# Performance work log

Measured on AMD Instinct MI355X. Metric: run time of the kernel, lower is better.

## Reference

```python
import jax, jax.numpy as jnp
import numpy as np

B, S, D = 2, 2048, 1024
DIM_Q = DIM_V = 1024
N_HEAD = 16
NORM = 1.0 / np.sqrt(DIM_Q)


def setup_inputs() -> dict:
    key = jax.random.key(0)
    ks = jax.random.split(key, 12)
    inp = {
        'q': jax.random.normal(ks[0], (B, S, D), jnp.float32),
        'k': jax.random.normal(ks[1], (B, S, D), jnp.float32),
        'v': jax.random.normal(ks[2], (B, S, D), jnp.float32),
        'attn_mask': jnp.zeros((1, 1, S, S), jnp.float32),
        # Linear weights stored torch-style: (out_features, in_features)
        'wq_w': jax.random.normal(ks[3], (DIM_Q, D), jnp.float32) * 0.02,
        'wq_b': jnp.zeros((DIM_Q,), jnp.float32),
        'wk_w': jax.random.normal(ks[4], (DIM_Q, D), jnp.float32) * 0.02,
        'wk_b': jnp.zeros((DIM_Q,), jnp.float32),
        'wv_w': jax.random.normal(ks[5], (DIM_V, D), jnp.float32) * 0.02,
        'wv_b': jnp.zeros((DIM_V,), jnp.float32),
        'wo_w': jax.random.normal(ks[6], (DIM_V, DIM_V), jnp.float32) * 0.02,
        'wo_b': jnp.zeros((DIM_V,), jnp.float32),
    }
    return inp


def reference(q, k, v, attn_mask, wq_w, wq_b, wk_w, wk_b, wv_w, wv_b, wo_w, wo_b):
    dh_k = DIM_Q // N_HEAD
    dh_v = DIM_V // N_HEAD
    Q = q @ wq_w.T + wq_b                     # [B,S,DQ]
    K = k @ wk_w.T + wk_b                     # [B,S,DQ]
    V = v @ wv_w.T + wv_b                     # [B,S,DV]
    # Faithful to the original: raw reshape (no transpose) to [B, H, S, dh]
    Q = Q.reshape(B, N_HEAD, S, dh_k)
    K = K.reshape(B, N_HEAD, S, dh_k)
    V = V.reshape(B, N_HEAD, S, dh_v)
    att = jnp.einsum('bhqd,bhkd->bhqk', Q, K) * NORM
    att = att + attn_mask
    att = jax.nn.softmax(att, axis=-1)        # dropout is identity (eval)
    out = jnp.einsum('bhqk,bhkd->bhqd', att, V).reshape(B, S, DIM_V)
    out = out @ wo_w.T + wo_b                 # [B,S,DV]
    return out
```

## Files before the change

### kernel.cpp

```cpp
#include <hip/hip_runtime.h>
#include <stdint.h>

#define S_LEN 2048
#define DMODEL 1024
#define DH 64
#define MROWS 4096
#define NORM 0.03125f
#define QSCALE 0.045084439f

typedef __bf16 bf16x8 __attribute__((ext_vector_type(8)));
typedef float f32x4 __attribute__((ext_vector_type(4)));
typedef float f32x16 __attribute__((ext_vector_type(16)));

__device__ __forceinline__ uint16_t f2bf(float f) {
  union { float f; uint32_t u; } c; c.f = f;
  uint32_t u = c.u;
  u += 0x7fffu + ((u >> 16) & 1u);
  return (uint16_t)(u >> 16);
}

__device__ __forceinline__ void gload_lds16(const void* g, void* l) {
  __builtin_amdgcn_global_load_lds(
      (__attribute__((address_space(1))) void*)g,
      (__attribute__((address_space(3))) void*)l, 16, 0, 0);
}

struct CvtArgs {
  const float* src[7];
  uint16_t* dst[7];
  float scale[7];
  int n[7];
};

__global__ void cvt_bf16_kernel(CvtArgs a) {
  const int y = blockIdx.y;
  const float* __restrict__ src = a.src[y];
  uint16_t* __restrict__ dst = a.dst[y];
  const float sc = a.scale[y];
  const int n = a.n[y];
  int i = (blockIdx.x * blockDim.x + threadIdx.x) * 4;
  const int stride = gridDim.x * blockDim.x * 4;
  for (; i < n; i += stride) {
    float4 f = *reinterpret_cast<const float4*>(src + i);
    ushort4 o;
    o.x = f2bf(f.x * sc); o.y = f2bf(f.y * sc); o.z = f2bf(f.z * sc); o.w = f2bf(f.w * sc);
    *reinterpret_cast<ushort4*>(dst + i) = o;
  }
}

struct GemmBatch {
  const uint16_t* A[3];
  const uint16_t* W[3];
  const float* bias[3];
  float bscale[3];
  void* C[3];
};

template <bool OUT_F32, int NBT>
__global__ __launch_bounds__(256) void gemm_bt_kernel(GemmBatch args, int K) {
  const int BN = 32 * NBT;
  const int z = blockIdx.z;
  const uint16_t* __restrict__ A = args.A[z];
  const uint16_t* __restrict__ W = args.W[z];
  const float* __restrict__ bias = args.bias[z];
  const float bsc = args.bscale[z];

  __shared__ uint16_t Al[2][128 * 32];
  __shared__ uint16_t Bl[2][32 * NBT * 32];

  const int tid = threadIdx.x;
  const int w = tid >> 6, l = tid & 63;
  const int wm = w >> 1, wn = w & 1;
  const int li = l & 15, lg = l >> 4;
  const int m0 = blockIdx.y * 128, n0 = blockIdx.x * BN;

  const f32x4 zero4 = {0.f, 0.f, 0.f, 0.f};
  f32x4 acc[4][NBT];
#pragma unroll
  for (int mt = 0; mt < 4; ++mt)
#pragma unroll
    for (int nt = 0; nt < NBT; ++nt) acc[mt][nt] = zero4;

  const int srow = l >> 2;
  const int sc = (l & 3) * 8;

  const int nsteps = K >> 5;

  {
    const uint16_t* Ag = A + (size_t)m0 * K;
    const uint16_t* Wg = W + (size_t)n0 * K;
#pragma unroll
    for (int i = 0; i < 2; ++i) {
      const int rr = (w * 2 + i) * 16 + srow;
      gload_lds16(Ag + (size_t)rr * K + sc, &Al[0][(w * 2 + i) * 512]);
    }
#pragma unroll
    for (int i = 0; i < BN / 64; ++i) {
      const int rr = (w * (BN / 64) + i) * 16 + srow;
      gload_lds16(Wg + (size_t)rr * K + sc, &Bl[0][(w * (BN / 64) + i) * 512]);
    }
  }
  __syncthreads();

#pragma unroll 2
  for (int kt = 0; kt < nsteps; ++kt) {
    const int cur = kt & 1;
    if (kt + 1 < nsteps) {
      const uint16_t* Ag = A + (size_t)m0 * K + (kt + 1) * 32;
      const uint16_t* Wg = W + (size_t)n0 * K + (kt + 1) * 32;
#pragma unroll
      for (int i = 0; i < 2; ++i) {
        const int rr = (w * 2 + i) * 16 + srow;
        gload_lds16(Ag + (size_t)rr * K + sc, &Al[cur ^ 1][(w * 2 + i) * 512]);
      }
#pragma unroll
      for (int i = 0; i < BN / 64; ++i) {
        const int rr = (w * (BN / 64) + i) * 16 + srow;
        gload_lds16(Wg + (size_t)rr * K + sc, &Bl[cur ^ 1][(w * (BN / 64) + i) * 512]);
      }
    }

    bf16x8 af[4], bfv[NBT];
#pragma unroll
    for (int mt = 0; mt < 4; ++mt)
      af[mt] = *reinterpret_cast<const bf16x8*>(&Al[cur][(wm * 64 + mt * 16 + li) * 32 + lg * 8]);
#pragma unroll
    for (int nt = 0; nt < NBT; ++nt)
      bfv[nt] = *reinterpret_cast<const bf16x8*>(&Bl[cur][(wn * (NBT * 16) + nt * 16 + li) * 32 + lg * 8]);
#pragma unroll
    for (int mt = 0; mt < 4; ++mt)
#pragma unroll
      for (int nt = 0; nt < NBT; ++nt)
        acc[mt][nt] = __builtin_amdgcn_mfma_f32_16x16x32_bf16(af[mt], bfv[nt], acc[mt][nt], 0, 0, 0);
    __syncthreads();
  }

  const int rowbase = m0 + wm * 64;
  const int colbase = n0 + wn * (NBT * 16);
#pragma unroll
  for (int nt = 0; nt < NBT; ++nt) {
    const int col = colbase + nt * 16 + li;
    const float bv = bias[col] * bsc;
#pragma unroll
    for (int mt = 0; mt < 4; ++mt) {
#pragma unroll
      for (int r = 0; r < 4; ++r) {
        const int row = rowbase + mt * 16 + lg * 4 + r;
        const float v = acc[mt][nt][r] + bv;
        if constexpr (OUT_F32)
          reinterpret_cast<float*>(args.C[z])[(size_t)row * DMODEL + col] = v;
        else
          reinterpret_cast<uint16_t*>(args.C[z])[(size_t)row * DMODEL + col] = f2bf(v);
      }
    }
  }
}

__global__ __launch_bounds__(256) void vt_kernel(const uint16_t* __restrict__ Vp,
                                                 uint16_t* __restrict__ VT) {
  const int chunk = blockIdx.y;
  const int kt = blockIdx.x;
  const size_t cbase = (size_t)chunk * (S_LEN * DH);
  __shared__ uint16_t T[64 * 72];

  const int tid = threadIdx.x;
  const int r = tid >> 2;
  const int c0 = (tid & 3) * 16;
#pragma unroll
  for (int e = 0; e < 2; ++e) {
    uint4 d = *reinterpret_cast<const uint4*>(Vp + cbase + (size_t)(kt * 64 + r) * DH + c0 + e * 8);
    *reinterpret_cast<uint4*>(&T[r * 72 + c0 + e * 8]) = d;
  }
  __syncthreads();
  const int wd = tid >> 2;
  const int kk0 = (tid & 3) * 16;
#pragma unroll
  for (int e = 0; e < 2; ++e) {
    union { uint4 u; uint16_t s[8]; } o;
#pragma unroll
    for (int j = 0; j < 8; ++j) o.s[j] = T[(kk0 + e * 8 + j) * 72 + wd];
    *reinterpret_cast<uint4*>(VT + cbase + (size_t)wd * S_LEN + kt * 64 + kk0 + e * 8) = o.u;
  }
}

__global__ __launch_bounds__(512, 4) void attn_kernel(const uint16_t* __restrict__ Qp,
                                                      const uint16_t* __restrict__ Kp,
                                                      const uint16_t* __restrict__ VT,
                                                      uint16_t* __restrict__ AO) {
  const int bh = blockIdx.y;
  const int qt = blockIdx.x;
  const size_t cbase = (size_t)bh * (S_LEN * DH);
  const uint16_t* Qc = Qp + cbase;
  const char* Kc = (const char*)(Kp + cbase);
  const char* VTc = (const char*)(VT + cbase);
  uint16_t* Oc = AO + cbase;

  __shared__ uint16_t KVl[4][32 * 128];
  __shared__ float Sm[4][32];
  __shared__ float Lsb[4][32];

  const int tid = threadIdx.x;
  const int w = tid >> 6, l = tid & 63;
  const int wq = w & 3, wk = w >> 2;
  const int col = l & 31, hi = l >> 5;

  const int qbase = qt * 128 + wq * 32;
  bf16x8 qf[4];
#pragma unroll
  for (int dm = 0; dm < 4; ++dm)
    qf[dm] = *reinterpret_cast<const bf16x8*>(
        Qc + (size_t)(qbase + col) * DH + dm * 16 + hi * 8);

  const int t = col >> 2;
  const int tt = (((t & 3) == 1) || ((t & 3) == 2)) ? (t ^ 3) : t;
  const int prow = (col & 3) | (tt << 2);

  int kfOff[4], vfOff[2][2];
  {
    const int k = wk * 32 + prow;
    const int row2 = k >> 1;
#pragma unroll
    for (int dm = 0; dm < 4; ++dm) {
      const int slot = (((k & 1) << 3) | (dm * 2 + hi)) ^ (row2 & 15);
      kfOff[dm] = row2 * 256 + slot * 16;
    }
#pragma unroll
    for (int ct = 0; ct < 2; ++ct) {
      const int d = ct * 32 + col;
      const int row2d = d >> 1;
#pragma unroll
      for (int kl = 0; kl < 2; ++kl) {
        const int ks = wk * 2 + kl;
        const int slot = (((d & 1) << 3) | (ks * 2 + hi)) ^ (row2d & 15);
        vfOff[kl][ct] = row2d * 256 + slot * 16;
      }
    }
  }

  int srcK, srcV;
  {
    const int o = (w << 10) + l * 16;
    const int row2 = o >> 8;
    const int su = ((o >> 4) & 15) ^ (row2 & 15);
    const int elem = row2 * 2 + (su >> 3);
    const int cb = (su & 7) * 16;
    srcK = elem * 128 + cb;
    srcV = elem * (S_LEN * 2) + cb;
  }

  f32x16 oacc[2];
#pragma unroll
  for (int b = 0; b < 2; ++b)
#pragma unroll
    for (int r = 0; r < 16; ++r) oacc[b][r] = 0.f;
  float ls = 0.f;

  gload_lds16(Kc + srcK, (char*)KVl[0] + (w << 10));
  gload_lds16(VTc + srcV, (char*)KVl[2] + (w << 10));
  __syncthreads();

#pragma unroll 2
  for (int kt = 0; kt < S_LEN / 64; ++kt) {
    const int cur = kt & 1;
    if (kt < S_LEN / 64 - 1) {
      gload_lds16(Kc + (size_t)(kt + 1) * (64 * DH * 2) + srcK,
                  (char*)KVl[cur ^ 1] + (w << 10));
      gload_lds16(VTc + srcV + (kt + 1) * 128,
                  (char*)KVl[2 + (cur ^ 1)] + (w << 10));
    }
    const char* Kb = (const char*)KVl[cur];
    const char* Vb = (const char*)KVl[2 + cur];

    bf16x8 kf[4];
#pragma unroll
    for (int dm = 0; dm < 4; ++dm)
      kf[dm] = *reinterpret_cast<const bf16x8*>(Kb + kfOff[dm]);
    bf16x8 vf[2][2];
#pragma unroll
    for (int kl = 0; kl < 2; ++kl)
#pragma unroll
      for (int ct = 0; ct < 2; ++ct)
        vf[kl][ct] = *reinterpret_cast<const bf16x8*>(Vb + vfOff[kl][ct]);

    f32x16 sacc;
#pragma unroll
    for (int r = 0; r < 16; ++r) sacc[r] = 0.f;
    __builtin_amdgcn_s_setprio(1);
#pragma unroll
    for (int dm = 0; dm < 4; ++dm)
      sacc = __builtin_amdgcn_mfma_f32_32x32x16_bf16(kf[dm], qf[dm], sacc, 0, 0, 0);
    __builtin_amdgcn_s_setprio(0);

    float e[16];
    float acc = 0.f;
#pragma unroll
    for (int r = 0; r < 16; ++r) { e[r] = __builtin_amdgcn_exp2f(sacc[r]); acc += e[r]; }
    ls += acc;
    union { __bf16 b[8]; bf16x8 v; } a0, a1;
#pragma unroll
    for (int i = 0; i < 8; ++i) { a0.b[i] = (__bf16)e[i]; a1.b[i] = (__bf16)e[8 + i]; }

    __builtin_amdgcn_s_setprio(1);
#pragma unroll
    for (int ct = 0; ct < 2; ++ct)
      oacc[ct] = __builtin_amdgcn_mfma_f32_32x32x16_bf16(a0.v, vf[0][ct], oacc[ct], 0, 0, 0);
#pragma unroll
    for (int ct = 0; ct < 2; ++ct)
      oacc[ct] = __builtin_amdgcn_mfma_f32_32x32x16_bf16(a1.v, vf[1][ct], oacc[ct], 0, 0, 0);
    __builtin_amdgcn_s_setprio(0);

    __syncthreads();
  }

  float* mbuf = (float*)KVl;
  const float tot_half = ls + __shfl_xor(ls, 32);
  if (wk == 1) {
    if (hi == 0) Lsb[wq][col] = tot_half;
#pragma unroll
    for (int ct = 0; ct < 2; ++ct)
#pragma unroll
      for (int r = 0; r < 16; ++r)
        mbuf[wq * 2048 + (ct * 16 + r) * 64 + l] = oacc[ct][r];
  }
  __syncthreads();
  if (wk == 0) {
    const float tot = tot_half + Lsb[wq][col];
    const float inv = 1.0f / tot;
    if (hi == 0) Sm[wq][col] = inv;
    f32x4 iv4[4];
#pragma unroll
    for (int g = 0; g < 4; ++g)
      iv4[g] = *reinterpret_cast<const f32x4*>(&Sm[wq][g * 8 + hi * 4]);
#pragma unroll
    for (int ct = 0; ct < 2; ++ct)
#pragma unroll
      for (int r = 0; r < 16; ++r) {
        const int q = qbase + (r & 3) + 8 * (r >> 2) + 4 * hi;
        const float v = oacc[ct][r] + mbuf[wq * 2048 + (ct * 16 + r) * 64 + l];
        Oc[(size_t)q * DH + ct * 32 + col] = f2bf(v * iv4[r >> 2][r & 3]);
      }
  }
}

extern "C" void kernel_launch(void* const* d_in, const int* in_sizes, int n_in,
                              void* d_out, int out_size, void* d_ws, size_t ws_size,
                              hipStream_t stream) {
  (void)in_sizes; (void)n_in; (void)out_size; (void)ws_size;
  const float* q    = (const float*)d_in[0];
  const float* k    = (const float*)d_in[1];
  const float* v    = (const float*)d_in[2];
  const float* wq_w = (const float*)d_in[4];
  const float* wq_b = (const float*)d_in[5];
  const float* wk_w = (const float*)d_in[6];
  const float* wk_b = (const float*)d_in[7];
  const float* wv_w = (const float*)d_in[8];
  const float* wv_b = (const float*)d_in[9];
  const float* wo_w = (const float*)d_in[10];
  const float* wo_b = (const float*)d_in[11];

  const size_t SZQ = (size_t)MROWS * DMODEL;
  const size_t SZW = (size_t)DMODEL * DMODEL;

  uint16_t* ws  = (uint16_t*)d_ws;
  uint16_t* qb  = ws;
  uint16_t* kb  = qb + SZQ;
  uint16_t* vb  = kb + SZQ;
  uint16_t* wqb = vb + SZQ;
  uint16_t* wkb = wqb + SZW;
  uint16_t* wvb = wkb + SZW;
  uint16_t* wob = wvb + SZW;
  uint16_t* Qp  = wob + SZW;
  uint16_t* Kp  = Qp + SZQ;
  uint16_t* Vp  = Kp + SZQ;
  uint16_t* AO  = Vp + SZQ;
  uint16_t* VTp = qb;

  CvtArgs ca;
  const float* srcs[7] = {q, k, v, wq_w, wk_w, wv_w, wo_w};
  uint16_t* dsts[7]    = {qb, kb, vb, wqb, wkb, wvb, wob};
  for (int i = 0; i < 7; ++i) {
    ca.src[i] = srcs[i];
    ca.dst[i] = dsts[i];
    ca.scale[i] = (i == 3) ? QSCALE : 1.0f;
    ca.n[i]   = (i < 3) ? (int)SZQ : (int)SZW;
  }
  cvt_bf16_kernel<<<dim3(512, 7), 256, 0, stream>>>(ca);

  GemmBatch g1;
  g1.A[0] = qb;  g1.A[1] = kb;  g1.A[2] = vb;
  g1.W[0] = wqb; g1.W[1] = wkb; g1.W[2] = wvb;
  g1.bias[0] = wq_b; g1.bias[1] = wk_b; g1.bias[2] = wv_b;
  g1.bscale[0] = QSCALE; g1.bscale[1] = 1.f; g1.bscale[2] = 1.f;
  g1.C[0] = Qp; g1.C[1] = Kp; g1.C[2] = Vp;
  gemm_bt_kernel<false, 4><<<dim3(8, 32, 3), 256, 0, stream>>>(g1, DMODEL);

  vt_kernel<<<dim3(32, 32), 256, 0, stream>>>(Vp, VTp);

  attn_kernel<<<dim3(16, 32), 512, 0, stream>>>(Qp, Kp, VTp, AO);

  GemmBatch g2;
  for (int i = 0; i < 3; ++i) {
    g2.A[i] = AO; g2.W[i] = wob; g2.bias[i] = wo_b; g2.bscale[i] = 1.f; g2.C[i] = d_out;
  }
  gemm_bt_kernel<true, 2><<<dim3(16, 32, 1), 256, 0, stream>>>(g2, DMODEL);
}
```

Measured before the change: 124.8 us.

## Split attention over two key halves with atomic fp32 partial merge

Adds a split over the key sequence (grid z=2) so each attention block handles half the key tiles, doubling the number of blocks to raise CU occupancy. Each split atomically adds its unnormalised fp32 output and row sums into zeroed scratch. A new merge kernel then normalises and converts the result to bf16. In exchange it adds a 16MB memset, fp32 atomic traffic and an extra kernel launch.

After: 157.5 us. 26.1% more time.

```diff
diff --git a/kernel.cpp b/kernel.cpp
--- a/kernel.cpp
+++ b/kernel.cpp
@@ -186,17 +186,18 @@
 __global__ __launch_bounds__(512, 4) void attn_kernel(const uint16_t* __restrict__ Qp,
                                                       const uint16_t* __restrict__ Kp,
                                                       const uint16_t* __restrict__ VT,
-                                                      uint16_t* __restrict__ AO) {
+                                                      float* __restrict__ Pp,
+                                                      float* __restrict__ Ls) {
   const int bh = blockIdx.y;
   const int qt = blockIdx.x;
+  const int ks = blockIdx.z;
   const size_t cbase = (size_t)bh * (S_LEN * DH);
   const uint16_t* Qc = Qp + cbase;
-  const char* Kc = (const char*)(Kp + cbase);
-  const char* VTc = (const char*)(VT + cbase);
-  uint16_t* Oc = AO + cbase;
+  const char* Kc = (const char*)(Kp + cbase) + (size_t)ks * 16 * 8192;
+  const char* VTc = (const char*)(VT + cbase) + ks * 2048;
+  const int NT = 16;
 
   __shared__ uint16_t KVl[4][32 * 128];
-  __shared__ float Sm[4][32];
   __shared__ float Lsb[4][32];
 
   const int tid = threadIdx.x;
@@ -230,8 +231,8 @@
       const int row2d = d >> 1;
 #pragma unroll
       for (int kl = 0; kl < 2; ++kl) {
-        const int ks = wk * 2 + kl;
-        const int slot = (((d & 1) << 3) | (ks * 2 + hi)) ^ (row2d & 15);
+        const int ksl = wk * 2 + kl;
+        const int slot = (((d & 1) << 3) | (ksl * 2 + hi)) ^ (row2d & 15);
         vfOff[kl][ct] = row2d * 256 + slot * 16;
       }
     }
@@ -260,10 +261,10 @@
   __syncthreads();
 
 #pragma unroll 2
-  for (int kt = 0; kt < S_LEN / 64; ++kt) {
+  for (int kt = 0; kt < NT; ++kt) {
     const int cur = kt & 1;
-    if (kt < S_LEN / 64 - 1) {
-      gload_lds16(Kc + (size_t)(kt + 1) * (64 * DH * 2) + srcK,
+    if (kt < NT - 1) {
+      gload_lds16(Kc + (size_t)(kt + 1) * 8192 + srcK,
                   (char*)KVl[cur ^ 1] + (w << 10));
       gload_lds16(VTc + srcV + (kt + 1) * 128,
                   (char*)KVl[2 + (cur ^ 1)] + (w << 10));
@@ -325,21 +326,29 @@
   __syncthreads();
   if (wk == 0) {
     const float tot = tot_half + Lsb[wq][col];
-    const float inv = 1.0f / tot;
-    if (hi == 0) Sm[wq][col] = inv;
-    f32x4 iv4[4];
-#pragma unroll
-    for (int g = 0; g < 4; ++g)
-      iv4[g] = *reinterpret_cast<const f32x4*>(&Sm[wq][g * 8 + hi * 4]);
+    if (hi == 0) atomicAdd(&Ls[(size_t)bh * S_LEN + qbase + col], tot);
+    float* Pc = Pp + (size_t)bh * (S_LEN * DH);
 #pragma unroll
     for (int ct = 0; ct < 2; ++ct)
 #pragma unroll
       for (int r = 0; r < 16; ++r) {
         const int q = qbase + (r & 3) + 8 * (r >> 2) + 4 * hi;
         const float v = oacc[ct][r] + mbuf[wq * 2048 + (ct * 16 + r) * 64 + l];
-        Oc[(size_t)q * DH + ct * 32 + col] = f2bf(v * iv4[r >> 2][r & 3]);
+        atomicAdd(&Pc[(size_t)q * DH + ct * 32 + col], v);
       }
   }
+}
+
+__global__ __launch_bounds__(256) void attn_merge_kernel(const float* __restrict__ Pp,
+                                                         const float* __restrict__ Ls,
+                                                         uint16_t* __restrict__ AO) {
+  const int i = blockIdx.x * blockDim.x + threadIdx.x;
+  const float4 p = reinterpret_cast<const float4*>(Pp)[i];
+  const float inv = 1.0f / Ls[i >> 4];
+  ushort4 o;
+  o.x = f2bf(p.x * inv); o.y = f2bf(p.y * inv);
+  o.z = f2bf(p.z * inv); o.w = f2bf(p.w * inv);
+  reinterpret_cast<ushort4*>(AO)[i] = o;
 }
 
 extern "C" void kernel_launch(void* const* d_in, const int* in_sizes, int n_in,
@@ -375,6 +384,9 @@
   uint16_t* AO  = Vp + SZQ;
   uint16_t* VTp = qb;
 
+  float* Pp = (float*)kb;
+  float* Ls = (float*)wqb;
+
   CvtArgs ca;
   const float* srcs[7] = {q, k, v, wq_w, wk_w, wv_w, wo_w};
   uint16_t* dsts[7]    = {qb, kb, vb, wqb, wkb, wvb, wob};
@@ -396,7 +408,11 @@
 
   vt_kernel<<<dim3(32, 32), 256, 0, stream>>>(Vp, VTp);
 
-  attn_kernel<<<dim3(16, 32), 512, 0, stream>>>(Qp, Kp, VTp, AO);
+  hipMemsetAsync(Pp, 0, (size_t)MROWS * DH * 32 / 2 * sizeof(float) + (size_t)MROWS * 16 * sizeof(float), stream);
+
+  attn_kernel<<<dim3(16, 32, 2), 512, 0, stream>>>(Qp, Kp, VTp, Pp, Ls);
+
+  attn_merge_kernel<<<dim3((MROWS * 16 * DH) / 4 / 256), 256, 0, stream>>>(Pp, Ls, AO);
 
   GemmBatch g2;
   for (int i = 0; i < 3; ++i) {
```
